# Kernel optimization log

Measured on AMD Instinct MI355X. Metric: run time of the kernel, lower is better.

## Reference

```python
import math
import jax, jax.numpy as jnp
import numpy as np

N = 4096
E = 131072
IN_C, HID_C, OUT_C = 128, 256, 128
RATIOS = (0.8, 0.6)


def _dense_adj(edge_index, n):
    # coalesced COO -> dense: duplicate edges sum (matches spspmm coalescing)
    A = jnp.zeros((n, n), jnp.float32)
    return A.at[edge_index[1], edge_index[0]].add(1.0)


def _augment(A):
    # add_self_loops(w=1) -> spspmm(A, A) -> remove_self_loops
    n = A.shape[0]
    eye = jnp.eye(n, dtype=A.dtype)
    A = A + eye
    A = A @ A
    return A * (1.0 - eye)


def _gcn(x, A, W, b):
    # GCNConv(improved=True): self-loop weight 2, sym normalization
    n = A.shape[0]
    Ah = A + 2.0 * jnp.eye(n, dtype=A.dtype)
    deg = Ah.sum(axis=1)
    dinv = jnp.where(deg > 0, deg ** -0.5, 0.0)
    An = dinv[:, None] * Ah * dinv[None, :]
    return An @ (x @ W) + b


def _topk_pool(x, A, w, ratio):
    score = jnp.tanh((x @ w) / jnp.linalg.norm(w))
    k = int(math.ceil(ratio * x.shape[0]))  # static
    vals, perm = jax.lax.top_k(score, k)
    x = x[perm] * vals[:, None]
    A = A[perm][:, perm]
    return x, A


def setup_inputs() -> dict:
    key = jax.random.key(0)
    ks = jax.random.split(key, 12)
    s = 0.05
    return {
        "x": jax.random.normal(ks[0], (N, IN_C), jnp.float32),
        "edge_index": jax.random.randint(ks[1], (2, E), 0, N, jnp.int32),
        "W0": jax.random.normal(ks[2], (IN_C, HID_C), jnp.float32) * s,
        "b0": jnp.zeros((HID_C,), jnp.float32),
        "W1": jax.random.normal(ks[3], (HID_C, HID_C), jnp.float32) * s,
        "b1": jnp.zeros((HID_C,), jnp.float32),
        "W2": jax.random.normal(ks[4], (HID_C, HID_C), jnp.float32) * s,
        "b2": jnp.zeros((HID_C,), jnp.float32),
        "p1": jax.random.normal(ks[5], (HID_C,), jnp.float32) * s,
        "p2": jax.random.normal(ks[6], (HID_C,), jnp.float32) * s,
        "Wout": jax.random.normal(ks[7], (HID_C, OUT_C), jnp.float32) * s,
        "bout": jnp.zeros((OUT_C,), jnp.float32),
    }


def reference(x, edge_index, W0, b0, W1, b1, W2, b2, p1, p2, Wout, bout):
    A = _dense_adj(edge_index, x.shape[0])
    A = _augment(A)
    x = jax.nn.relu(_gcn(x, A, W0, b0))
    # dropout p=0.5 -> identity (inference)
    for (W, b, p, r) in ((W1, b1, p1, RATIOS[0]), (W2, b2, p2, RATIOS[1])):
        A = _augment(A)
        x, A = _topk_pool(x, A, p, r)
        x = jax.nn.relu(_gcn(x, A, W, b))
    x = _gcn(x, A, Wout, bout)
    batch = jnp.zeros((x.shape[0],), jnp.int32)
    return x, batch
```

## Files before the change

### kernel.cpp

```cpp
#include <hip/hip_runtime.h>
#include <math.h>

#define N0    4096
#define CIN   128
#define HID   256
#define COUTC 128
#define K1P   3277
#define K2P   1967
#define LD3   1968
#define KI2   3328
#define KI3   1984
#define DNUM  5

typedef __attribute__((ext_vector_type(4))) int i32x4;

__device__ __forceinline__ void gl2lds16(const void* g, void* l) {
  __builtin_amdgcn_global_load_lds((const __attribute__((address_space(1))) void*)g,
                                   (__attribute__((address_space(3))) void*)l, 16, 0, 0);
}


__global__ void k_zero32(float* __restrict__ p, size_t n) {
  size_t i = (size_t)blockIdx.x * blockDim.x + threadIdx.x;
  size_t st = (size_t)gridDim.x * blockDim.x;
  for (; i < n; i += st) p[i] = 0.0f;
}

__global__ void k_widen_f32_f64(const float* __restrict__ in, double* __restrict__ out, int n) {
  int i = blockIdx.x * blockDim.x + threadIdx.x;
  int st = gridDim.x * blockDim.x;
  for (; i < n; i += st) out[i] = (double)in[i];
}

__global__ void k_build_adj(const int* __restrict__ ei, float* __restrict__ A, int E, int n) {
  int e = blockIdx.x * blockDim.x + threadIdx.x;
  if (e < E) atomicAdd(&A[(size_t)ei[E + e] * n + ei[e]], 1.0f);
}

__global__ __launch_bounds__(256) void k_transpose_split_i8(
    const float* __restrict__ A, char* __restrict__ B, char* __restrict__ BT) {
  __shared__ char sm[64][68];
  const int t = threadIdx.x;
  const int r0 = blockIdx.y * 64, c0 = blockIdx.x * 64;
  const int rr = t >> 2, cs = (t & 3) * 16;
  char tmp[16];
#pragma unroll
  for (int j = 0; j < 16; ++j) {
    char v = (char)(int)A[(size_t)(r0 + rr) * N0 + c0 + cs + j];
    tmp[j] = v;
    sm[cs + j][rr] = v;
  }
  *(int4*)&B[(size_t)(r0 + rr) * N0 + c0 + cs] = *(int4*)&tmp[0];
  __syncthreads();
  const int cc = t >> 2, rs = (t & 3) * 16;
  const int orow = c0 + cc;
  char o[16];
#pragma unroll
  for (int q = 0; q < 16; ++q) {
    char v = sm[cc][rs + q];
    if (r0 + rs + q == orow) v = (char)(v + 2);
    o[q] = v;
  }
  *(int4*)&BT[(size_t)orow * N0 + r0 + rs] = *(int4*)&o[0];
}

__global__ __launch_bounds__(256) void k_transpose_i8s(
    const char* __restrict__ A, char* __restrict__ BT, int n, int fold) {
  __shared__ char sm[64][68];
  const int t = threadIdx.x;
  const int r0 = blockIdx.y * 64, c0 = blockIdx.x * 64;
  const int rr = t >> 2, cs = (t & 3) * 16;
  {
    int4 v = *(const int4*)&A[(size_t)(r0 + rr) * n + c0 + cs];
    char* vb = (char*)&v;
#pragma unroll
    for (int j = 0; j < 16; ++j) sm[cs + j][rr] = vb[j];
  }
  __syncthreads();
  const int cc = t >> 2, rs = (t & 3) * 16;
  const int orow = c0 + cc;
  char o[16];
#pragma unroll
  for (int q = 0; q < 16; ++q) {
    char v = sm[cc][rs + q];
    if (r0 + rs + q == orow) v = (char)(v + fold);
    o[q] = v;
  }
  *(int4*)&BT[(size_t)orow * n + r0 + rs] = *(int4*)&o[0];
}

template <int MODE>
__global__ __launch_bounds__(256) void k_aug_pipe8(
    const char* __restrict__ Asrc, const char* __restrict__ Btsrc,
    const int* __restrict__ perm, const char* __restrict__ zrow,
    int K, int ldk,
    char* __restrict__ O, size_t plane, int ldo,
    int M, int N)
{
  __shared__ __align__(16) char Ls[2][2][8192];
  const int tid = threadIdx.x;
  const int wave = tid >> 6, lane = tid & 63;
  const int wr = wave >> 1, wc = wave & 1;
  const int brow = blockIdx.y * 128, bcol = blockIdx.x * 128;
  const int lr = lane & 15, ko = (lane >> 4) * 16;
  const int koff = (lane & 3) * 16;

  const char* pA[2];
  const char* pB[2];
#pragma unroll
  for (int c = 0; c < 2; ++c) {
    int r = (c * 4 + wave) * 16 + (lane >> 2);
    int ra = brow + r, rb = bcol + r;
    int ia, ib;
    if (MODE == 0) { ia = ra; ib = rb; }
    else {
      ia = (ra < M) ? perm[ra] : -1;
      ib = (rb < N) ? perm[rb] : -1;
    }
    pA[c] = (ia >= 0) ? Asrc + (size_t)ia * ldk : zrow;
    pB[c] = (ib >= 0) ? Btsrc + (size_t)ib * ldk : zrow;
  }

  i32x4 acc[4][4];
#pragma unroll
  for (int m = 0; m < 4; ++m)
#pragma unroll
    for (int n = 0; n < 4; ++n) acc[m][n] = (i32x4){0, 0, 0, 0};

  auto STAGE = [&](int buf, int kt) {
#pragma unroll
    for (int c = 0; c < 2; ++c) {
      int f = c * 4 + wave;
      gl2lds16(pA[c] + kt + koff, &Ls[buf][0][f * 1024]);
      gl2lds16(pB[c] + kt + koff, &Ls[buf][1][f * 1024]);
    }
  };

  STAGE(0, 0);
  __syncthreads();
  int cur = 0;
  for (int kt = 0; kt < K; kt += 64) {
    if (kt + 64 < K) STAGE(cur ^ 1, kt + 64);
    i32x4 a0[4], b0[4];
#pragma unroll
    for (int m = 0; m < 4; ++m) a0[m] = *(const i32x4*)&Ls[cur][0][(wr * 64 + m * 16 + lr) * 64 + ko];
#pragma unroll
    for (int n = 0; n < 4; ++n) b0[n] = *(const i32x4*)&Ls[cur][1][(wc * 64 + n * 16 + lr) * 64 + ko];
#pragma unroll
    for (int m = 0; m < 4; ++m)
#pragma unroll
      for (int n = 0; n < 4; ++n)
        acc[m][n] = __builtin_amdgcn_mfma_i32_16x16x64_i8(a0[m], b0[n], acc[m][n], 0, 0, 0);
    __syncthreads();
    cur ^= 1;
  }

#pragma unroll
  for (int m = 0; m < 4; ++m)
#pragma unroll
    for (int n = 0; n < 4; ++n)
#pragma unroll
      for (int q = 0; q < 4; ++q) {
        int grow = brow + wr * 64 + m * 16 + (lane >> 4) * 4 + q;
        int gcol = bcol + wc * 64 + n * 16 + lr;
        int v = acc[m][n][q];
        if (MODE == 0) {
          if (grow == gcol) v = 0;
          O[(size_t)grow * ldo + gcol] = (char)v;
        } else {
          if (grow >= M || gcol >= N || grow == gcol) v = 0;
          O[(size_t)grow * ldo + gcol] = (char)(v >> 7);
          O[plane + (size_t)grow * ldo + gcol] = (char)(v & 127);
        }
      }
}

__global__ __launch_bounds__(512) void k_aug3_pipe8(
    const char* __restrict__ S, const char* __restrict__ ST,
    const int* __restrict__ perm, const char* __restrict__ zrow,
    int Kpad, float* __restrict__ Cf, unsigned* __restrict__ amax,
    int M, int N, int ldcp)
{
  __shared__ __align__(16) char Ls[2][4][8192];
  const int tid = threadIdx.x;
  const int wave = tid >> 6, lane = tid & 63;
  const int wr = wave >> 1, wc = wave & 1;
  const int brow = blockIdx.y * 128, bcol = blockIdx.x * 128;
  const int lr = lane & 15, ko = (lane >> 4) * 16;
  const int koff = (lane & 3) * 16;
  const size_t plane = (size_t)Kpad * Kpad;

  const char *pAh, *pAl, *pBh, *pBl;
  {
    int r = (wave << 4) + (lane >> 2);
    int ra = brow + r, rb = bcol + r;
    int ia = (ra < M) ? perm[ra] : -1;
    int ib = (rb < N) ? perm[rb] : -1;
    pAh = (ia >= 0) ? S + (size_t)ia * Kpad : zrow;
    pAl = (ia >= 0) ? S + plane + (size_t)ia * Kpad : zrow;
    pBh = (ib >= 0) ? ST + (size_t)ib * Kpad : zrow;
    pBl = (ib >= 0) ? ST + plane + (size_t)ib * Kpad : zrow;
  }

  i32x4 hh[2][4], mid[2][4];
#pragma unroll
  for (int m = 0; m < 2; ++m)
#pragma unroll
    for (int n = 0; n < 4; ++n) {
      hh[m][n] = (i32x4){0, 0, 0, 0};
      mid[m][n] = (i32x4){0, 0, 0, 0};
    }

  auto STAGE = [&](int buf, int kt) {
    int f = wave * 1024;
    gl2lds16(pAh + kt + koff, &Ls[buf][0][f]);
    gl2lds16(pBh + kt + koff, &Ls[buf][1][f]);
    gl2lds16(pAl + kt + koff, &Ls[buf][2][f]);
    gl2lds16(pBl + kt + koff, &Ls[buf][3][f]);
  };

  STAGE(0, 0);
  __syncthreads();
  int cur = 0;
  for (int kt = 0; kt < Kpad; kt += 64) {
    if (kt + 64 < Kpad) STAGE(cur ^ 1, kt + 64);
    i32x4 ah[2], al[2], bh[4], bl[4];
#pragma unroll
    for (int m = 0; m < 2; ++m) {
      ah[m] = *(const i32x4*)&Ls[cur][0][(wr * 32 + m * 16 + lr) * 64 + ko];
      al[m] = *(const i32x4*)&Ls[cur][2][(wr * 32 + m * 16 + lr) * 64 + ko];
    }
#pragma unroll
    for (int n = 0; n < 4; ++n) {
      bh[n] = *(const i32x4*)&Ls[cur][1][(wc * 64 + n * 16 + lr) * 64 + ko];
      bl[n] = *(const i32x4*)&Ls[cur][3][(wc * 64 + n * 16 + lr) * 64 + ko];
    }
#pragma unroll
    for (int m = 0; m < 2; ++m)
#pragma unroll
      for (int n = 0; n < 4; ++n) {
        hh[m][n]  = __builtin_amdgcn_mfma_i32_16x16x64_i8(ah[m], bh[n], hh[m][n], 0, 0, 0);
        mid[m][n] = __builtin_amdgcn_mfma_i32_16x16x64_i8(ah[m], bl[n], mid[m][n], 0, 0, 0);
        mid[m][n] = __builtin_amdgcn_mfma_i32_16x16x64_i8(al[m], bh[n], mid[m][n], 0, 0, 0);
      }
    __syncthreads();
    cur ^= 1;
  }

  float mloc = 0.0f;
#pragma unroll
  for (int m = 0; m < 2; ++m)
#pragma unroll
    for (int n = 0; n < 4; ++n)
#pragma unroll
      for (int q = 0; q < 4; ++q) {
        int grow = brow + wr * 32 + m * 16 + (lane >> 4) * 4 + q;
        int gcol = bcol + wc * 64 + n * 16 + lr;
        if (grow < M && gcol < ldcp) {
          float v = 16384.0f * (float)hh[m][n][q] + 128.0f * (float)mid[m][n][q];
          if (gcol >= N || grow == gcol) v = 0.0f;
          Cf[(size_t)grow * ldcp + gcol] = v;
          mloc = fmaxf(mloc, v);
        }
      }
  __syncthreads();
  float* red = (float*)&Ls[0][0][0];
  red[tid] = mloc;
  __syncthreads();
  for (int st = 256; st > 0; st >>= 1) {
    if (tid < st) red[tid] = fmaxf(red[tid], red[tid + st]);
    __syncthreads();
  }
  if (tid == 0) atomicMax(amax, __builtin_bit_cast(unsigned, red[0]));
}


__global__ __launch_bounds__(256) void k_gemm_xw32(
    const double* __restrict__ X, const float* __restrict__ W, double* __restrict__ C,
    int M, int N, int K, unsigned* __restrict__ rst) {
  if (blockIdx.x == 0 && blockIdx.y == 0 && threadIdx.x == 0 && threadIdx.y == 0 && rst) *rst = 0u;
  __shared__ double As[16][32];
  __shared__ double Bs[16][64];
  const int tx = threadIdx.x, ty = threadIdx.y;
  const int tid = ty * 16 + tx;
  const int brow = blockIdx.y * 32, bcol = blockIdx.x * 64;
  double acc[2][4];
#pragma unroll
  for (int i = 0; i < 2; ++i)
#pragma unroll
    for (int j = 0; j < 4; ++j) acc[i][j] = 0.0;
  const int lac = tid & 15, lar = tid >> 4;
  const int lbc = tid & 63, lbr = tid >> 6;
  for (int kt = 0; kt < K; kt += 16) {
#pragma unroll
    for (int rr = 0; rr < 2; ++rr) {
      int r = lar + rr * 16;
      int gr = brow + r, gk = kt + lac;
      As[lac][r] = (gr < M && gk < K) ? X[(size_t)gr * K + gk] : 0.0;
    }
#pragma unroll
    for (int rr = 0; rr < 4; ++rr) {
      int br = lbr + rr * 4;
      int gk = kt + br, gc = bcol + lbc;
      Bs[br][lbc] = (gk < K && gc < N) ? (double)W[(size_t)gk * N + gc] : 0.0;
    }
    __syncthreads();
#pragma unroll
    for (int kk = 0; kk < 16; ++kk) {
      double a[2], b[4];
#pragma unroll
      for (int i = 0; i < 2; ++i) a[i] = As[kk][ty * 2 + i];
#pragma unroll
      for (int j = 0; j < 4; ++j) b[j] = Bs[kk][tx * 4 + j];
#pragma unroll
      for (int i = 0; i < 2; ++i)
#pragma unroll
        for (int j = 0; j < 4; ++j) acc[i][j] = fma(a[i], b[j], acc[i][j]);
    }
    __syncthreads();
  }
#pragma unroll
  for (int i = 0; i < 2; ++i) {
    int gr = brow + ty * 2 + i;
    if (gr >= M) continue;
#pragma unroll
    for (int j = 0; j < 4; ++j) {
      int gc = bcol + tx * 4 + j;
      if (gc >= N) continue;
      C[(size_t)gr * N + gc] = acc[i][j];
    }
  }
}


__global__ void k_wmax(const double* __restrict__ t, const double* __restrict__ dinv,
                       unsigned* __restrict__ wmax, int K, int N) {
  __shared__ float red[256];
  float mx = 0.0f;
  int tot = K * N;
  for (int i = blockIdx.x * 256 + threadIdx.x; i < tot; i += gridDim.x * 256) {
    double w = dinv[i / N] * t[i];
    mx = fmaxf(mx, (float)fabs(w));
  }
  red[threadIdx.x] = mx;
  __syncthreads();
  for (int st = 128; st > 0; st >>= 1) {
    if (threadIdx.x < st) red[threadIdx.x] = fmaxf(red[threadIdx.x], red[threadIdx.x + st]);
    __syncthreads();
  }
  if (threadIdx.x == 0) atomicMax(wmax, __builtin_bit_cast(unsigned, red[0]));
}

template <int D>
__global__ __launch_bounds__(256) void k_digitize8(
    const double* __restrict__ t, const double* __restrict__ dinv,
    const unsigned* __restrict__ wmax, char* __restrict__ wdT,
    int K, int Kpad, int N) {
  __shared__ char sm[D][64][68];
  const int tid = threadIdx.x;
  const int k0 = blockIdx.x * 64, n0 = blockIdx.y * 64;
  float wm = __builtin_bit_cast(float, *wmax);
  double sc = (wm > 0.0f) ? scalbn(1.0, -(ilogbf(wm) + 2)) : 0.0;
  const int kk = tid >> 2, ns = (tid & 3) * 16;
  int k = k0 + kk;
  double dv = (k < K) ? dinv[k] : 0.0;
#pragma unroll
  for (int j = 0; j < 16; ++j) {
    int n = n0 + ns + j;
    double w = (k < K) ? dv * t[(size_t)k * N + n] : 0.0;
    double r = w * sc;
#pragma unroll
    for (int d = 0; d < D; ++d) {
      double rm = r * 128.0;
      double m = rint(rm);
      sm[d][kk][ns + j] = (char)(int)m;
      r = rm - m;
    }
  }
  __syncthreads();
  const int nn = tid >> 2, ks = (tid & 3) * 16;
  const size_t PS = (size_t)N * Kpad;
#pragma unroll
  for (int d = 0; d < D; ++d) {
    char o[16];
#pragma unroll
    for (int j = 0; j < 16; ++j) o[j] = sm[d][ks + j][nn];
    *(int4*)&wdT[d * PS + (size_t)(n0 + nn) * Kpad + k0 + ks] = *(int4*)&o[0];
  }
}

__global__ void k_splitA8s(const float* __restrict__ A, int M, int ldsrc,
                           const unsigned* __restrict__ amax,
                           char* __restrict__ S, int Kpad) {
  int r = blockIdx.x;
  const size_t plane = (size_t)Kpad * Kpad;
  float am = __builtin_bit_cast(float, *amax);
  float s13 = (am > 0.0f) ? scalbnf(1.0f, 13 - (ilogbf(am) + 1)) : 0.0f;
  for (int c4 = threadIdx.x * 4; c4 < Kpad; c4 += blockDim.x * 4) {
    float v[4] = {0.f, 0.f, 0.f, 0.f};
    if (r < M && c4 < ldsrc) *(float4*)v = *(const float4*)(A + (size_t)r * ldsrc + c4);
    unsigned hw = 0, lw = 0;
#pragma unroll
    for (int q = 0; q < 4; ++q) {
      int iv = (int)rintf(v[q] * s13);
      int h = iv >> 7, l = iv - (h << 7);
      hw |= ((unsigned)(unsigned char)(char)h) << (8 * q);
      lw |= ((unsigned)(unsigned char)(char)l) << (8 * q);
    }
    *(unsigned*)(S + (size_t)r * Kpad + c4) = hw;
    *(unsigned*)(S + plane + (size_t)r * Kpad + c4) = lw;
  }
}

__global__ __launch_bounds__(256) void k_axw_pipe8(
    const char* __restrict__ Asrc, const char* __restrict__ Bsrc,
    int Kpad, int* __restrict__ P, int Neff)
{
  __shared__ __align__(16) char Ls[2][2][8192];
  const int tid = threadIdx.x;
  const int wave = tid >> 6, lane = tid & 63;
  const int wr = wave >> 1, wc = wave & 1;
  const int brow = blockIdx.y * 128, bcol = blockIdx.x * 128;
  const int lr = lane & 15, ko = (lane >> 4) * 16;
  const int koff = (lane & 3) * 16;

  const char* pA[2];
  const char* pB[2];
#pragma unroll
  for (int c = 0; c < 2; ++c) {
    int r = (c * 4 + wave) * 16 + (lane >> 2);
    pA[c] = Asrc + (size_t)(brow + r) * Kpad;
    pB[c] = Bsrc + (size_t)(bcol + r) * Kpad;
  }

  i32x4 acc[4][4];
#pragma unroll
  for (int m = 0; m < 4; ++m)
#pragma unroll
    for (int n = 0; n < 4; ++n) acc[m][n] = (i32x4){0, 0, 0, 0};

  auto STAGE = [&](int buf, int kt) {
#pragma unroll
    for (int c = 0; c < 2; ++c) {
      int f = c * 4 + wave;
      gl2lds16(pA[c] + kt + koff, &Ls[buf][0][f * 1024]);
      gl2lds16(pB[c] + kt + koff, &Ls[buf][1][f * 1024]);
    }
  };

  STAGE(0, 0);
  __syncthreads();
  int cur = 0;
  for (int kt = 0; kt < Kpad; kt += 64) {
    if (kt + 64 < Kpad) STAGE(cur ^ 1, kt + 64);
    i32x4 a0[4], b0[4];
#pragma unroll
    for (int m = 0; m < 4; ++m) a0[m] = *(const i32x4*)&Ls[cur][0][(wr * 64 + m * 16 + lr) * 64 + ko];
#pragma unroll
    for (int n = 0; n < 4; ++n) b0[n] = *(const i32x4*)&Ls[cur][1][(wc * 64 + n * 16 + lr) * 64 + ko];
#pragma unroll
    for (int m = 0; m < 4; ++m)
#pragma unroll
      for (int n = 0; n < 4; ++n)
        acc[m][n] = __builtin_amdgcn_mfma_i32_16x16x64_i8(a0[m], b0[n], acc[m][n], 0, 0, 0);
    __syncthreads();
    cur ^= 1;
  }

#pragma unroll
  for (int m = 0; m < 4; ++m)
#pragma unroll
    for (int n = 0; n < 4; ++n)
#pragma unroll
      for (int q = 0; q < 4; ++q) {
        int grow = brow + wr * 64 + m * 16 + (lane >> 4) * 4 + q;
        int gcol = bcol + wc * 64 + n * 16 + lr;
        P[(size_t)grow * Neff + gcol] = acc[m][n][q];
      }
}

__global__ void k_reduce_fin(const int* __restrict__ P, const unsigned* __restrict__ wmax,
                             const unsigned* __restrict__ amax,
                             const double* __restrict__ t, const double* __restrict__ dinv,
                             const float* __restrict__ bias, double* __restrict__ out,
                             int Neff, int N, int D, int M0pad, int nplane,
                             double w0, double w1, int relu) {
  int m = blockIdx.x;
  float wm = __builtin_bit_cast(float, *wmax);
  double s0 = w0, s1 = w1;
  bool zero = (wm <= 0.0f);
  if (amax) {
    float am = __builtin_bit_cast(float, *amax);
    if (am > 0.0f) {
      int EA = ilogbf(am) + 1;
      s0 = scalbn(w0, EA - 13);
      s1 = scalbn(w1, EA - 13);
    } else zero = true;
  }
  int Ep = zero ? 0 : (ilogbf(wm) + 2);
  double d = dinv[m];
  for (int n = threadIdx.x; n < N; n += blockDim.x) {
    double acc = 0.0;
    if (!zero) {
      for (int dd = 0; dd < D; ++dd) {
        double v = s0 * (double)P[(size_t)m * Neff + dd * N + n];
        if (nplane == 2) v += s1 * (double)P[(size_t)(M0pad + m) * Neff + dd * N + n];
        acc += scalbn(v, Ep - 7 * (dd + 1));
      }
    }
    double v = d * (acc + 2.0 * d * t[(size_t)m * N + n]) + (double)bias[n];
    if (relu) v = v > 0.0 ? v : 0.0;
    out[(size_t)m * N + n] = v;
  }
}


template <typename TA>
__device__ __forceinline__ float a_as_f32(TA v);
template <> __device__ __forceinline__ float a_as_f32<char>(char v) { return (float)v; }
template <> __device__ __forceinline__ float a_as_f32<float>(float v) { return v; }

template <typename TA>
__global__ void k_degdinv(const TA* __restrict__ A, int lda, double* __restrict__ dinv, int n,
                          unsigned* __restrict__ rst0, unsigned* __restrict__ rst1) {
  if (blockIdx.x == 0 && threadIdx.x == 0) {
    if (rst0) *rst0 = 0u;
    if (rst1) *rst1 = 0u;
  }
  __shared__ double red[256];
  int row = blockIdx.x;
  double s = 0.0;
  for (int j = threadIdx.x; j < n; j += 256) s += (double)a_as_f32<TA>(A[(size_t)row * lda + j]);
  red[threadIdx.x] = s;
  __syncthreads();
  for (int st = 128; st > 0; st >>= 1) {
    if (threadIdx.x < st) red[threadIdx.x] += red[threadIdx.x + st];
    __syncthreads();
  }
  if (threadIdx.x == 0) {
    double deg = red[0] + 2.0;
    dinv[row] = (deg > 0.0) ? 1.0 / sqrt(deg) : 0.0;
  }
}

__global__ void k_degdinv2p(const char* __restrict__ S, int Kpad, double* __restrict__ dinv,
                            int n, unsigned* __restrict__ rst0) {
  if (blockIdx.x == 0 && threadIdx.x == 0 && rst0) *rst0 = 0u;
  __shared__ double red[256];
  const size_t plane = (size_t)Kpad * Kpad;
  int row = blockIdx.x;
  const char* h = S + (size_t)row * Kpad;
  const char* l = S + plane + (size_t)row * Kpad;
  long s = 0;
  for (int j = threadIdx.x; j < n; j += 256) s += 128 * (long)h[j] + (long)l[j];
  red[threadIdx.x] = (double)s;
  __syncthreads();
  for (int st = 128; st > 0; st >>= 1) {
    if (threadIdx.x < st) red[threadIdx.x] += red[threadIdx.x + st];
    __syncthreads();
  }
  if (threadIdx.x == 0) {
    double deg = red[0] + 2.0;
    dinv[row] = (deg > 0.0) ? 1.0 / sqrt(deg) : 0.0;
  }
}

__global__ void k_scores(const double* __restrict__ x, const float* __restrict__ p,
                         double* __restrict__ sc, int C, unsigned* __restrict__ rst) {
  if (blockIdx.x == 0 && threadIdx.x == 0 && rst) *rst = 0u;
  __shared__ double red[256], red2[256];
  int row = blockIdx.x;
  double s = 0.0, s2 = 0.0;
  for (int j = threadIdx.x; j < C; j += 256) {
    double pv = (double)p[j];
    s += x[(size_t)row * C + j] * pv;
    s2 += pv * pv;
  }
  red[threadIdx.x] = s;
  red2[threadIdx.x] = s2;
  __syncthreads();
  for (int st = 128; st > 0; st >>= 1) {
    if (threadIdx.x < st) {
      red[threadIdx.x] += red[threadIdx.x + st];
      red2[threadIdx.x] += red2[threadIdx.x + st];
    }
    __syncthreads();
  }
  if (threadIdx.x == 0) sc[row] = tanh(red[0] / sqrt(red2[0]));
}

__global__ __launch_bounds__(256) void k_topk_rank(
    const double* __restrict__ sc, int n, int k,
    int* __restrict__ perm, double* __restrict__ vals) {
  __shared__ int red[256];
  const int i = blockIdx.x;
  const double si = sc[i];
  int cnt = 0;
  for (int j = threadIdx.x; j < n; j += 256) {
    double sj = sc[j];
    if (sj > si || (sj == si && j < i)) ++cnt;
  }
  red[threadIdx.x] = cnt;
  __syncthreads();
  for (int st = 128; st > 0; st >>= 1) {
    if (threadIdx.x < st) red[threadIdx.x] += red[threadIdx.x + st];
    __syncthreads();
  }
  if (threadIdx.x == 0) {
    int rank = red[0];
    if (rank < k) { perm[rank] = i; vals[rank] = si; }
  }
}

__global__ void k_gather_x(const double* __restrict__ x, const int* __restrict__ perm,
                           const double* __restrict__ vals, double* __restrict__ xo, int C) {
  int row = blockIdx.x;
  int src = perm[row];
  double v = vals[row];
  for (int c = threadIdx.x; c < C; c += blockDim.x)
    xo[(size_t)row * C + c] = x[(size_t)src * C + c] * v;
}

__global__ void k_write_out(const double* __restrict__ x, float* __restrict__ out,
                            int nvals, int total) {
  int i = blockIdx.x * blockDim.x + threadIdx.x;
  int st = gridDim.x * blockDim.x;
  for (; i < total; i += st) out[i] = (i < nvals) ? (float)x[i] : 0.0f;
}

__global__ void k_sentinel(float* __restrict__ out, int total) {
  int i = blockIdx.x * blockDim.x + threadIdx.x;
  int st = gridDim.x * blockDim.x;
  for (; i < total; i += st) out[i] = 1e30f;
}


extern "C" void kernel_launch(void* const* d_in, const int* in_sizes, int n_in,
                              void* d_out, int out_size, void* d_ws, size_t ws_size,
                              hipStream_t stream) {
  const float* x0f  = (const float*)d_in[0];
  const int*   ei   = (const int*)d_in[1];
  const float* W0   = (const float*)d_in[2];
  const float* b0   = (const float*)d_in[3];
  const float* W1   = (const float*)d_in[4];
  const float* b1   = (const float*)d_in[5];
  const float* W2   = (const float*)d_in[6];
  const float* b2   = (const float*)d_in[7];
  const float* p1   = (const float*)d_in[8];
  const float* p2   = (const float*)d_in[9];
  const float* Wout = (const float*)d_in[10];
  const float* bout = (const float*)d_in[11];
  const int E = in_sizes[1] / 2;

  const size_t MiB = 1ull << 20;
  if (ws_size < 160 * MiB) {
    k_sentinel<<<dim3(256), dim3(256), 0, stream>>>((float*)d_out, out_size);
    return;
  }
  char* W = (char*)d_ws;
  const size_t PL2 = (size_t)KI2 * KI2;
  float* A0    = (float*)(W + 0);
  char*  A0s8  = (char*)(W + 64 * MiB);
  char*  A0s8T = (char*)(W + 80 * MiB);
  char*  A1    = (char*)(W + 0);
  char*  A1T   = (char*)(W + 16 * MiB);
  char*  wdT1  = (char*)(W + 32 * MiB);
  int*   P1    = (int*)(W + 40 * MiB);
  char*  A2s8  = (char*)(W + 64 * MiB);
  char*  A2s8T = (char*)(W + 86 * MiB);
  char*  wdT2  = (char*)(W + 0);
  int*   P2    = (int*)(W + 7 * MiB);
  float* A3p     = (float*)(W + 108 * MiB);
  char*  A3stack = (char*)(W + 0);
  char*  wdT3    = (char*)(W + 8 * MiB);
  int*   P3      = (int*)(W + 10 * MiB);
  double* tb   = (double*)(W + 128 * MiB);
  double* xA   = (double*)(W + 144 * MiB);
  double* xB   = (double*)(W + 152 * MiB);
  char* SM = W + (159 * MiB + 256 * 1024);
  double* dinv = (double*)(SM);
  double* sc   = (double*)(SM + 32768);
  double* vals = (double*)(SM + 65536);
  unsigned* wmax  = (unsigned*)(SM + 98304 + 128);
  unsigned* a3max = (unsigned*)(SM + 98304 + 192);
  int* perm    = (int*)(SM + 98304 + 256);
  int* permB   = (int*)(SM + 98304 + 256 + 16384);
  char* zpage  = (char*)(W + 159 * MiB + 512 * 1024);

  k_zero32<<<dim3(8), dim3(256), 0, stream>>>((float*)zpage, 8192);
  k_zero32<<<dim3(2048), dim3(256), 0, stream>>>(A0, (size_t)N0 * N0);
  k_build_adj<<<dim3((E + 255) / 256), dim3(256), 0, stream>>>(ei, A0, E, N0);
  k_transpose_split_i8<<<dim3(64, 64), dim3(256), 0, stream>>>(A0, A0s8, A0s8T);

  k_aug_pipe8<0><<<dim3(32, 32), dim3(256), 0, stream>>>(
      A0s8, A0s8T, nullptr, zpage, N0, N0, A1, 0, N0, N0, N0);
  k_transpose_i8s<<<dim3(64, 64), dim3(256), 0, stream>>>(A1, A1T, N0, 2);

  k_widen_f32_f64<<<dim3(512), dim3(256), 0, stream>>>(x0f, xB, N0 * CIN);
  {
    dim3 b(16, 16);
    k_gemm_xw32<<<dim3(HID / 64, (N0 + 31) / 32), b, 0, stream>>>(xB, W0, tb, N0, HID, CIN, nullptr);
    k_degdinv<char><<<dim3(N0), dim3(256), 0, stream>>>(A1, N0, dinv, N0, wmax, nullptr);
    k_wmax<<<dim3(256), dim3(256), 0, stream>>>(tb, dinv, wmax, N0, HID);
    k_digitize8<DNUM><<<dim3(N0 / 64, HID / 64), dim3(256), 0, stream>>>(tb, dinv, wmax, wdT1, N0, N0, HID);
    k_axw_pipe8<<<dim3(DNUM * HID / 128, N0 / 128), dim3(256), 0, stream>>>(A1, wdT1, N0, P1, DNUM * HID);
    k_reduce_fin<<<dim3(N0), dim3(256), 0, stream>>>(P1, wmax, nullptr, tb, dinv, b0, xA,
                                                     DNUM * HID, HID, DNUM, 0, 1, 1.0, 0.0, 1);
  }

  k_scores<<<dim3(N0), dim3(256), 0, stream>>>(xA, p1, sc, HID, nullptr);
  k_topk_rank<<<dim3(N0), dim3(256), 0, stream>>>(sc, N0, K1P, perm, vals);
  k_gather_x<<<dim3(K1P), dim3(256), 0, stream>>>(xA, perm, vals, xB, HID);

  k_aug_pipe8<1><<<dim3(26, 26), dim3(256), 0, stream>>>(
      A1, A1T, perm, zpage, N0, N0, A2s8, PL2, KI2, K1P, K1P);
  k_transpose_i8s<<<dim3(52, 52), dim3(256), 0, stream>>>(A2s8, A2s8T, KI2, 0);
  k_transpose_i8s<<<dim3(52, 52), dim3(256), 0, stream>>>(A2s8 + PL2, A2s8T + PL2, KI2, 2);

  {
    dim3 b(16, 16);
    k_gemm_xw32<<<dim3(HID / 64, (K1P + 31) / 32), b, 0, stream>>>(xB, W1, tb, K1P, HID, HID, nullptr);
    k_degdinv2p<<<dim3(K1P), dim3(256), 0, stream>>>(A2s8, KI2, dinv, K1P, wmax);
    k_wmax<<<dim3(256), dim3(256), 0, stream>>>(tb, dinv, wmax, K1P, HID);
    k_digitize8<DNUM><<<dim3(KI2 / 64, HID / 64), dim3(256), 0, stream>>>(tb, dinv, wmax, wdT2, K1P, KI2, HID);
    k_axw_pipe8<<<dim3(DNUM * HID / 128, 2 * KI2 / 128), dim3(256), 0, stream>>>(A2s8, wdT2, KI2, P2, DNUM * HID);
    k_reduce_fin<<<dim3(K1P), dim3(256), 0, stream>>>(P2, wmax, nullptr, tb, dinv, b1, xA,
                                                      DNUM * HID, HID, DNUM, KI2, 2, 128.0, 1.0, 1);
  }

  k_scores<<<dim3(K1P), dim3(256), 0, stream>>>(xA, p2, sc, HID, a3max);
  k_topk_rank<<<dim3(K1P), dim3(256), 0, stream>>>(sc, K1P, K2P, permB, vals);
  k_gather_x<<<dim3(K2P), dim3(256), 0, stream>>>(xA, permB, vals, xB, HID);

  k_aug3_pipe8<<<dim3(16, 16), dim3(512), 0, stream>>>(
      A2s8, A2s8T, permB, zpage, KI2, A3p, a3max, K2P, K2P, LD3);

  {
    dim3 b(16, 16);
    k_gemm_xw32<<<dim3(HID / 64, (K2P + 31) / 32), b, 0, stream>>>(xB, W2, tb, K2P, HID, HID, nullptr);
    k_degdinv<float><<<dim3(K2P), dim3(256), 0, stream>>>(A3p, LD3, dinv, K2P, wmax, nullptr);
    k_splitA8s<<<dim3(KI3), dim3(256), 0, stream>>>(A3p, K2P, LD3, a3max, A3stack, KI3);
    k_wmax<<<dim3(256), dim3(256), 0, stream>>>(tb, dinv, wmax, K2P, HID);
    k_digitize8<2><<<dim3(KI3 / 64, HID / 64), dim3(256), 0, stream>>>(tb, dinv, wmax, wdT3, K2P, KI3, HID);
    k_axw_pipe8<<<dim3(2 * HID / 128, 2 * KI3 / 128), dim3(256), 0, stream>>>(A3stack, wdT3, KI3, P3, 2 * HID);
    k_reduce_fin<<<dim3(K2P), dim3(256), 0, stream>>>(P3, wmax, a3max, tb, dinv, b2, xA,
                                                      2 * HID, HID, 2, KI3, 2, 128.0, 1.0, 1);
  }

  {
    dim3 b(16, 16);
    k_gemm_xw32<<<dim3(COUTC / 64, (K2P + 31) / 32), b, 0, stream>>>(xA, Wout, tb, K2P, COUTC, HID, wmax);
    k_wmax<<<dim3(256), dim3(256), 0, stream>>>(tb, dinv, wmax, K2P, COUTC);
    k_digitize8<2><<<dim3(KI3 / 64, COUTC / 64), dim3(256), 0, stream>>>(tb, dinv, wmax, wdT3, K2P, KI3, COUTC);
    k_axw_pipe8<<<dim3(2 * COUTC / 128, 2 * KI3 / 128), dim3(256), 0, stream>>>(A3stack, wdT3, KI3, P3, 2 * COUTC);
    k_reduce_fin<<<dim3(K2P), dim3(256), 0, stream>>>(P3, wmax, a3max, tb, dinv, bout, xB,
                                                      2 * COUTC, COUTC, 2, KI3, 2, 128.0, 1.0, 0);
  }

  k_write_out<<<dim3(1024), dim3(256), 0, stream>>>(xB, (float*)d_out, K2P * COUTC, out_size);
}
```

Measured before the change: 689.3 us.

## Build int8 adjacency directly and fuse scores, gather, widen, output into neighbors

The adjacency is built straight into packed int8 with byte-lane atomic adds, which removes the 64 MiB float matrix, its zeroing, and the float-to-int8 conversion pass. The node-score computation is folded into the reduce/finalize kernel. The top-k gather and scaling, and the f32-to-f64 widening of x, are folded into the XW GEMM's A-tile loads. The final float output write and padding zeroing move into the last finalize kernel, and the two plane transposes are merged into one z-indexed launch. The aim is fewer launches and less memory traffic; the packed byte atomics would wrap if any edge count reached 256.

```diff
diff --git a/kernel.cpp b/kernel.cpp
--- a/kernel.cpp
+++ b/kernel.cpp
@@ -26,52 +26,26 @@
   for (; i < n; i += st) p[i] = 0.0f;
 }
 
-__global__ void k_widen_f32_f64(const float* __restrict__ in, double* __restrict__ out, int n) {
-  int i = blockIdx.x * blockDim.x + threadIdx.x;
-  int st = gridDim.x * blockDim.x;
-  for (; i < n; i += st) out[i] = (double)in[i];
-}
-
-__global__ void k_build_adj(const int* __restrict__ ei, float* __restrict__ A, int E, int n) {
+__global__ void k_build_adj8(const int* __restrict__ ei, unsigned* __restrict__ A, int E, int n) {
   int e = blockIdx.x * blockDim.x + threadIdx.x;
-  if (e < E) atomicAdd(&A[(size_t)ei[E + e] * n + ei[e]], 1.0f);
-}
-
-__global__ __launch_bounds__(256) void k_transpose_split_i8(
-    const float* __restrict__ A, char* __restrict__ B, char* __restrict__ BT) {
+  if (e < E) {
+    size_t byte = (size_t)ei[E + e] * n + ei[e];
+    atomicAdd(&A[byte >> 2], 1u << (8 * (byte & 3)));
+  }
+}
+
+__global__ __launch_bounds__(256) void k_transpose_i8s(
+    const char* __restrict__ A, char* __restrict__ BT, int n, size_t splane,
+    int fold0, int fold1) {
   __shared__ char sm[64][68];
-  const int t = threadIdx.x;
-  const int r0 = blockIdx.y * 64, c0 = blockIdx.x * 64;
-  const int rr = t >> 2, cs = (t & 3) * 16;
-  char tmp[16];
-#pragma unroll
-  for (int j = 0; j < 16; ++j) {
-    char v = (char)(int)A[(size_t)(r0 + rr) * N0 + c0 + cs + j];
-    tmp[j] = v;
-    sm[cs + j][rr] = v;
-  }
-  *(int4*)&B[(size_t)(r0 + rr) * N0 + c0 + cs] = *(int4*)&tmp[0];
-  __syncthreads();
-  const int cc = t >> 2, rs = (t & 3) * 16;
-  const int orow = c0 + cc;
-  char o[16];
-#pragma unroll
-  for (int q = 0; q < 16; ++q) {
-    char v = sm[cc][rs + q];
-    if (r0 + rs + q == orow) v = (char)(v + 2);
-    o[q] = v;
-  }
-  *(int4*)&BT[(size_t)orow * N0 + r0 + rs] = *(int4*)&o[0];
-}
-
-__global__ __launch_bounds__(256) void k_transpose_i8s(
-    const char* __restrict__ A, char* __restrict__ BT, int n, int fold) {
-  __shared__ char sm[64][68];
+  const char* src = A + blockIdx.z * splane;
+  char* dst = BT + blockIdx.z * splane;
+  const int fold = blockIdx.z ? fold1 : fold0;
   const int t = threadIdx.x;
   const int r0 = blockIdx.y * 64, c0 = blockIdx.x * 64;
   const int rr = t >> 2, cs = (t & 3) * 16;
   {
-    int4 v = *(const int4*)&A[(size_t)(r0 + rr) * n + c0 + cs];
+    int4 v = *(const int4*)&src[(size_t)(r0 + rr) * n + c0 + cs];
     char* vb = (char*)&v;
 #pragma unroll
     for (int j = 0; j < 16; ++j) sm[cs + j][rr] = vb[j];
@@ -86,7 +60,7 @@
     if (r0 + rs + q == orow) v = (char)(v + fold);
     o[q] = v;
   }
-  *(int4*)&BT[(size_t)orow * n + r0 + rs] = *(int4*)&o[0];
+  *(int4*)&dst[(size_t)orow * n + r0 + rs] = *(int4*)&o[0];
 }
 
 template <int MODE>
@@ -275,8 +249,10 @@
 }
 
 
+template <typename TX, int GATHER>
 __global__ __launch_bounds__(256) void k_gemm_xw32(
-    const double* __restrict__ X, const float* __restrict__ W, double* __restrict__ C,
+    const TX* __restrict__ X, const int* __restrict__ perm, const double* __restrict__ vals,
+    const float* __restrict__ W, double* __restrict__ C,
     int M, int N, int K, unsigned* __restrict__ rst) {
   if (blockIdx.x == 0 && blockIdx.y == 0 && threadIdx.x == 0 && threadIdx.y == 0 && rst) *rst = 0u;
   __shared__ double As[16][32];
@@ -284,19 +260,40 @@
   const int tx = threadIdx.x, ty = threadIdx.y;
   const int tid = ty * 16 + tx;
   const int brow = blockIdx.y * 32, bcol = blockIdx.x * 64;
-  double acc[2][4];
-#pragma unroll
-  for (int i = 0; i < 2; ++i)
-#pragma unroll
-    for (int j = 0; j < 4; ++j) acc[i][j] = 0.0;
   const int lac = tid & 15, lar = tid >> 4;
   const int lbc = tid & 63, lbr = tid >> 6;
+
+  int srow[2];
+  double sval[2];
+#pragma unroll
+  for (int rr = 0; rr < 2; ++rr) {
+    int gr = brow + lar + rr * 16;
+    if (GATHER) {
+      srow[rr] = (gr < M) ? perm[gr] : 0;
+      sval[rr] = (gr < M) ? vals[gr] : 0.0;
+    } else {
+      srow[rr] = gr;
+      sval[rr] = 1.0;
+    }
+  }
+
+  double acc[2][4];
+#pragma unroll
+  for (int i = 0; i < 2; ++i)
+#pragma unroll
+    for (int j = 0; j < 4; ++j) acc[i][j] = 0.0;
+
   for (int kt = 0; kt < K; kt += 16) {
 #pragma unroll
     for (int rr = 0; rr < 2; ++rr) {
-      int r = lar + rr * 16;
-      int gr = brow + r, gk = kt + lac;
-      As[lac][r] = (gr < M && gk < K) ? X[(size_t)gr * K + gk] : 0.0;
+      int gr = brow + lar + rr * 16;
+      int gk = kt + lac;
+      double v = 0.0;
+      if (gr < M && gk < K) {
+        v = (double)X[(size_t)srow[rr] * K + gk];
+        if (GATHER) v *= sval[rr];
+      }
+      As[lac][lar + rr * 16] = v;
     }
 #pragma unroll
     for (int rr = 0; rr < 4; ++rr) {
@@ -479,13 +476,18 @@
       }
 }
 
+template <int SCORES, int OUT32>
 __global__ void k_reduce_fin(const int* __restrict__ P, const unsigned* __restrict__ wmax,
                              const unsigned* __restrict__ amax,
                              const double* __restrict__ t, const double* __restrict__ dinv,
                              const float* __restrict__ bias, double* __restrict__ out,
+                             float* __restrict__ fout, int nvals, int total,
+                             const float* __restrict__ p, double* __restrict__ scv,
+                             unsigned* __restrict__ rst,
                              int Neff, int N, int D, int M0pad, int nplane,
                              double w0, double w1, int relu) {
   int m = blockIdx.x;
+  if (SCORES) { if (m == 0 && threadIdx.x == 0 && rst) *rst = 0u; }
   float wm = __builtin_bit_cast(float, *wmax);
   double s0 = w0, s1 = w1;
   bool zero = (wm <= 0.0f);
@@ -499,6 +501,8 @@
   }
   int Ep = zero ? 0 : (ilogbf(wm) + 2);
   double d = dinv[m];
+  __shared__ double red[256], red2[256];
+  double sdot = 0.0, sp2 = 0.0;
   for (int n = threadIdx.x; n < N; n += blockDim.x) {
     double acc = 0.0;
     if (!zero) {
@@ -510,7 +514,30 @@
     }
     double v = d * (acc + 2.0 * d * t[(size_t)m * N + n]) + (double)bias[n];
     if (relu) v = v > 0.0 ? v : 0.0;
-    out[(size_t)m * N + n] = v;
+    if (OUT32) fout[(size_t)m * N + n] = (float)v;
+    else out[(size_t)m * N + n] = v;
+    if (SCORES) {
+      double pv = (double)p[n];
+      sdot += v * pv;
+      sp2 += pv * pv;
+    }
+  }
+  if (OUT32) {
+    if (m == 0)
+      for (int i = nvals + threadIdx.x; i < total; i += blockDim.x) fout[i] = 0.0f;
+  }
+  if (SCORES) {
+    red[threadIdx.x] = sdot;
+    red2[threadIdx.x] = sp2;
+    __syncthreads();
+    for (int st = 128; st > 0; st >>= 1) {
+      if (threadIdx.x < st) {
+        red[threadIdx.x] += red[threadIdx.x + st];
+        red2[threadIdx.x] += red2[threadIdx.x + st];
+      }
+      __syncthreads();
+    }
+    if (threadIdx.x == 0) scv[m] = tanh(red[0] / sqrt(red2[0]));
   }
 }
 
@@ -565,30 +592,6 @@
   }
 }
 
-__global__ void k_scores(const double* __restrict__ x, const float* __restrict__ p,
-                         double* __restrict__ sc, int C, unsigned* __restrict__ rst) {
-  if (blockIdx.x == 0 && threadIdx.x == 0 && rst) *rst = 0u;
-  __shared__ double red[256], red2[256];
-  int row = blockIdx.x;
-  double s = 0.0, s2 = 0.0;
-  for (int j = threadIdx.x; j < C; j += 256) {
-    double pv = (double)p[j];
-    s += x[(size_t)row * C + j] * pv;
-    s2 += pv * pv;
-  }
-  red[threadIdx.x] = s;
-  red2[threadIdx.x] = s2;
-  __syncthreads();
-  for (int st = 128; st > 0; st >>= 1) {
-    if (threadIdx.x < st) {
-      red[threadIdx.x] += red[threadIdx.x + st];
-      red2[threadIdx.x] += red2[threadIdx.x + st];
-    }
-    __syncthreads();
-  }
-  if (threadIdx.x == 0) sc[row] = tanh(red[0] / sqrt(red2[0]));
-}
-
 __global__ __launch_bounds__(256) void k_topk_rank(
     const double* __restrict__ sc, int n, int k,
     int* __restrict__ perm, double* __restrict__ vals) {
@@ -610,22 +613,6 @@
     int rank = red[0];
     if (rank < k) { perm[rank] = i; vals[rank] = si; }
   }
-}
-
-__global__ void k_gather_x(const double* __restrict__ x, const int* __restrict__ perm,
-                           const double* __restrict__ vals, double* __restrict__ xo, int C) {
-  int row = blockIdx.x;
-  int src = perm[row];
-  double v = vals[row];
-  for (int c = threadIdx.x; c < C; c += blockDim.x)
-    xo[(size_t)row * C + c] = x[(size_t)src * C + c] * v;
-}
-
-__global__ void k_write_out(const double* __restrict__ x, float* __restrict__ out,
-                            int nvals, int total) {
-  int i = blockIdx.x * blockDim.x + threadIdx.x;
-  int st = gridDim.x * blockDim.x;
-  for (; i < total; i += st) out[i] = (i < nvals) ? (float)x[i] : 0.0f;
 }
 
 __global__ void k_sentinel(float* __restrict__ out, int total) {
@@ -659,7 +646,6 @@
   }
   char* W = (char*)d_ws;
   const size_t PL2 = (size_t)KI2 * KI2;
-  float* A0    = (float*)(W + 0);
   char*  A0s8  = (char*)(W + 64 * MiB);
   char*  A0s8T = (char*)(W + 80 * MiB);
   char*  A1    = (char*)(W + 0);
@@ -676,7 +662,6 @@
   int*   P3      = (int*)(W + 10 * MiB);
   double* tb   = (double*)(W + 128 * MiB);
   double* xA   = (double*)(W + 144 * MiB);
-  double* xB   = (double*)(W + 152 * MiB);
   char* SM = W + (159 * MiB + 256 * 1024);
   double* dinv = (double*)(SM);
   double* sc   = (double*)(SM + 32768);
@@ -688,74 +673,74 @@
   char* zpage  = (char*)(W + 159 * MiB + 512 * 1024);
 
   k_zero32<<<dim3(8), dim3(256), 0, stream>>>((float*)zpage, 8192);
-  k_zero32<<<dim3(2048), dim3(256), 0, stream>>>(A0, (size_t)N0 * N0);
-  k_build_adj<<<dim3((E + 255) / 256), dim3(256), 0, stream>>>(ei, A0, E, N0);
-  k_transpose_split_i8<<<dim3(64, 64), dim3(256), 0, stream>>>(A0, A0s8, A0s8T);
+  k_zero32<<<dim3(1024), dim3(256), 0, stream>>>((float*)A0s8, (size_t)N0 * N0 / 4);
+  k_build_adj8<<<dim3((E + 255) / 256), dim3(256), 0, stream>>>(ei, (unsigned*)A0s8, E, N0);
+  k_transpose_i8s<<<dim3(64, 64, 1), dim3(256), 0, stream>>>(A0s8, A0s8T, N0, 0, 2, 0);
 
   k_aug_pipe8<0><<<dim3(32, 32), dim3(256), 0, stream>>>(
       A0s8, A0s8T, nullptr, zpage, N0, N0, A1, 0, N0, N0, N0);
-  k_transpose_i8s<<<dim3(64, 64), dim3(256), 0, stream>>>(A1, A1T, N0, 2);
-
-  k_widen_f32_f64<<<dim3(512), dim3(256), 0, stream>>>(x0f, xB, N0 * CIN);
+  k_transpose_i8s<<<dim3(64, 64, 1), dim3(256), 0, stream>>>(A1, A1T, N0, 0, 2, 0);
+
   {
     dim3 b(16, 16);
-    k_gemm_xw32<<<dim3(HID / 64, (N0 + 31) / 32), b, 0, stream>>>(xB, W0, tb, N0, HID, CIN, nullptr);
+    k_gemm_xw32<float, 0><<<dim3(HID / 64, (N0 + 31) / 32), b, 0, stream>>>(
+        x0f, nullptr, nullptr, W0, tb, N0, HID, CIN, nullptr);
     k_degdinv<char><<<dim3(N0), dim3(256), 0, stream>>>(A1, N0, dinv, N0, wmax, nullptr);
     k_wmax<<<dim3(256), dim3(256), 0, stream>>>(tb, dinv, wmax, N0, HID);
     k_digitize8<DNUM><<<dim3(N0 / 64, HID / 64), dim3(256), 0, stream>>>(tb, dinv, wmax, wdT1, N0, N0, HID);
     k_axw_pipe8<<<dim3(DNUM * HID / 128, N0 / 128), dim3(256), 0, stream>>>(A1, wdT1, N0, P1, DNUM * HID);
-    k_reduce_fin<<<dim3(N0), dim3(256), 0, stream>>>(P1, wmax, nullptr, tb, dinv, b0, xA,
-                                                     DNUM * HID, HID, DNUM, 0, 1, 1.0, 0.0, 1);
-  }
-
-  k_scores<<<dim3(N0), dim3(256), 0, stream>>>(xA, p1, sc, HID, nullptr);
+    k_reduce_fin<1, 0><<<dim3(N0), dim3(256), 0, stream>>>(
+        P1, wmax, nullptr, tb, dinv, b0, xA, nullptr, 0, 0, p1, sc, nullptr,
+        DNUM * HID, HID, DNUM, 0, 1, 1.0, 0.0, 1);
+  }
+
   k_topk_rank<<<dim3(N0), dim3(256), 0, stream>>>(sc, N0, K1P, perm, vals);
-  k_gather_x<<<dim3(K1P), dim3(256), 0, stream>>>(xA, perm, vals, xB, HID);
 
   k_aug_pipe8<1><<<dim3(26, 26), dim3(256), 0, stream>>>(
       A1, A1T, perm, zpage, N0, N0, A2s8, PL2, KI2, K1P, K1P);
-  k_transpose_i8s<<<dim3(52, 52), dim3(256), 0, stream>>>(A2s8, A2s8T, KI2, 0);
-  k_transpose_i8s<<<dim3(52, 52), dim3(256), 0, stream>>>(A2s8 + PL2, A2s8T + PL2, KI2, 2);
+  k_transpose_i8s<<<dim3(52, 52, 2), dim3(256), 0, stream>>>(A2s8, A2s8T, KI2, PL2, 0, 2);
 
   {
     dim3 b(16, 16);
-    k_gemm_xw32<<<dim3(HID / 64, (K1P + 31) / 32), b, 0, stream>>>(xB, W1, tb, K1P, HID, HID, nullptr);
+    k_gemm_xw32<double, 1><<<dim3(HID / 64, (K1P + 31) / 32), b, 0, stream>>>(
+        xA, perm, vals, W1, tb, K1P, HID, HID, nullptr);
     k_degdinv2p<<<dim3(K1P), dim3(256), 0, stream>>>(A2s8, KI2, dinv, K1P, wmax);
     k_wmax<<<dim3(256), dim3(256), 0, stream>>>(tb, dinv, wmax, K1P, HID);
     k_digitize8<DNUM><<<dim3(KI2 / 64, HID / 64), dim3(256), 0, stream>>>(tb, dinv, wmax, wdT2, K1P, KI2, HID);
     k_axw_pipe8<<<dim3(DNUM * HID / 128, 2 * KI2 / 128), dim3(256), 0, stream>>>(A2s8, wdT2, KI2, P2, DNUM * HID);
-    k_reduce_fin<<<dim3(K1P), dim3(256), 0, stream>>>(P2, wmax, nullptr, tb, dinv, b1, xA,
-                                                      DNUM * HID, HID, DNUM, KI2, 2, 128.0, 1.0, 1);
-  }
-
-  k_scores<<<dim3(K1P), dim3(256), 0, stream>>>(xA, p2, sc, HID, a3max);
+    k_reduce_fin<1, 0><<<dim3(K1P), dim3(256), 0, stream>>>(
+        P2, wmax, nullptr, tb, dinv, b1, xA, nullptr, 0, 0, p2, sc, a3max,
+        DNUM * HID, HID, DNUM, KI2, 2, 128.0, 1.0, 1);
+  }
+
   k_topk_rank<<<dim3(K1P), dim3(256), 0, stream>>>(sc, K1P, K2P, permB, vals);
-  k_gather_x<<<dim3(K2P), dim3(256), 0, stream>>>(xA, permB, vals, xB, HID);
 
   k_aug3_pipe8<<<dim3(16, 16), dim3(512), 0, stream>>>(
       A2s8, A2s8T, permB, zpage, KI2, A3p, a3max, K2P, K2P, LD3);
 
   {
     dim3 b(16, 16);
-    k_gemm_xw32<<<dim3(HID / 64, (K2P + 31) / 32), b, 0, stream>>>(xB, W2, tb, K2P, HID, HID, nullptr);
+    k_gemm_xw32<double, 1><<<dim3(HID / 64, (K2P + 31) / 32), b, 0, stream>>>(
+        xA, permB, vals, W2, tb, K2P, HID, HID, nullptr);
     k_degdinv<float><<<dim3(K2P), dim3(256), 0, stream>>>(A3p, LD3, dinv, K2P, wmax, nullptr);
     k_splitA8s<<<dim3(KI3), dim3(256), 0, stream>>>(A3p, K2P, LD3, a3max, A3stack, KI3);
     k_wmax<<<dim3(256), dim3(256), 0, stream>>>(tb, dinv, wmax, K2P, HID);
     k_digitize8<2><<<dim3(KI3 / 64, HID / 64), dim3(256), 0, stream>>>(tb, dinv, wmax, wdT3, K2P, KI3, HID);
     k_axw_pipe8<<<dim3(2 * HID / 128, 2 * KI3 / 128), dim3(256), 0, stream>>>(A3stack, wdT3, KI3, P3, 2 * HID);
-    k_reduce_fin<<<dim3(K2P), dim3(256), 0, stream>>>(P3, wmax, a3max, tb, dinv, b2, xA,
-                                                      2 * HID, HID, 2, KI3, 2, 128.0, 1.0, 1);
+    k_reduce_fin<0, 0><<<dim3(K2P), dim3(256), 0, stream>>>(
+        P3, wmax, a3max, tb, dinv, b2, xA, nullptr, 0, 0, nullptr, nullptr, nullptr,
+        2 * HID, HID, 2, KI3, 2, 128.0, 1.0, 1);
   }
 
   {
     dim3 b(16, 16);
-    k_gemm_xw32<<<dim3(COUTC / 64, (K2P + 31) / 32), b, 0, stream>>>(xA, Wout, tb, K2P, COUTC, HID, wmax);
+    k_gemm_xw32<double, 0><<<dim3(COUTC / 64, (K2P + 31) / 32), b, 0, stream>>>(
+        xA, nullptr, nullptr, Wout, tb, K2P, COUTC, HID, wmax);
     k_wmax<<<dim3(256), dim3(256), 0, stream>>>(tb, dinv, wmax, K2P, COUTC);
     k_digitize8<2><<<dim3(KI3 / 64, COUTC / 64), dim3(256), 0, stream>>>(tb, dinv, wmax, wdT3, K2P, KI3, COUTC);
     k_axw_pipe8<<<dim3(2 * COUTC / 128, 2 * KI3 / 128), dim3(256), 0, stream>>>(A3stack, wdT3, KI3, P3, 2 * COUTC);
-    k_reduce_fin<<<dim3(K2P), dim3(256), 0, stream>>>(P3, wmax, a3max, tb, dinv, bout, xB,
-                                                      2 * COUTC, COUTC, 2, KI3, 2, 128.0, 1.0, 0);
-  }
-
-  k_write_out<<<dim3(1024), dim3(256), 0, stream>>>(xB, (float*)d_out, K2P * COUTC, out_size);
-}
+    k_reduce_fin<0, 1><<<dim3(K2P), dim3(256), 0, stream>>>(
+        P3, wmax, a3max, tb, dinv, bout, nullptr, (float*)d_out, K2P * COUTC, out_size,
+        nullptr, nullptr, nullptr, 2 * COUTC, COUTC, 2, KI3, 2, 128.0, 1.0, 0);
+  }
+}
```

After: 653.2 us (median of 2 runs). -5.2%, faster.
